# Kernel tuning notes

Hardware: AMD Instinct MI355X
Metric: run time of the kernel (lower is better)

Reference implementation:

```python
import jax, jax.numpy as jnp
import numpy as np


def setup_inputs() -> dict:
    key = jax.random.key(0)
    ks = jax.random.split(key, 4)
    B, T, C, L, DQ = 8, 2048, 256, 32, 512
    return {
        "vis_feats": jax.random.normal(ks[0], (B, T, C), dtype=jnp.float32),
        "query": jax.random.normal(ks[1], (B, L, DQ), dtype=jnp.float32),
        "W1": jax.random.normal(ks[2], (DQ, C), dtype=jnp.float32) / np.float32(np.sqrt(DQ)),
        "b1": jnp.zeros((C,), dtype=jnp.float32),
        "W2": jax.random.normal(ks[3], (DQ, C), dtype=jnp.float32) / np.float32(np.sqrt(DQ)),
        "b2": jnp.zeros((C,), dtype=jnp.float32),
        "window_size": 32,
        "num_chunks": 8,
    }


def reference(vis_feats, query, W1, b1, W2, b2, window_size, num_chunks):
    B, T, C = vis_feats.shape
    L = query.shape[1]
    # seq encoders (modeled as linear projections): [B, L, C]
    enc1 = query @ W1 + b1
    enc2 = query @ W2 + b2
    # clip-word similarity and per-clip word label: [B, T]
    sim = jnp.einsum("btc,blc->btl", vis_feats, enc1)
    clip_labels = jnp.argmax(sim, axis=2)
    NW = T - window_size + 1
    cic = window_size // num_chunks  # clips per chunk
    # sliding-window unfold indices: [NW, window_size]
    idx = jnp.arange(NW)[:, None] + jnp.arange(window_size)[None, :]
    vis_unf = vis_feats[:, idx, :]                      # [B, NW, W, C]
    lab_unf = clip_labels[:, idx].reshape(B, NW, num_chunks, cic)
    # majority vote per chunk == argmax of label histogram (ties -> smallest label,
    # matching np.bincount + np.argmax)
    counts = jax.nn.one_hot(lab_unf, L, dtype=jnp.int32).sum(axis=3)  # [B, NW, K, L]
    lbls = jnp.argmax(counts, axis=-1)                  # [B, NW, K]
    # adaptive_avg_pool3d (K, cic, C) -> (K, 1, C) == mean over clips-in-chunk
    pooled = vis_unf.reshape(B, NW, num_chunks, cic, C).mean(axis=3)  # [B, NW, K, C]
    # gather the majority-vote word encoding and modulate
    gathered = enc2[jnp.arange(B)[:, None, None], lbls]  # [B, NW, K, C]
    return gathered * pooled
```

## Files before the change

kernel.cpp:

```cpp
#include <hip/hip_runtime.h>
#include <hip/hip_bf16.h>

#define B   8
#define T   2048
#define C   256
#define L   32
#define DQ  512
#define NW  2017
#define NK  8
#define CIC 4
#define WT  32
#define SROWS (WT + (NK-1)*CIC)

__global__ __launch_bounds__(256) void enc_kernel(
    const float* __restrict__ query, const float* __restrict__ W1,
    const float* __restrict__ b1, const float* __restrict__ W2,
    const float* __restrict__ b2, float* __restrict__ enc1,
    float* __restrict__ enc2) {
  const int b = blockIdx.y, lg = blockIdx.x;
  const int c = threadIdx.x;
  __shared__ float qs[4 * DQ];
  const float* qbase = query + ((size_t)b * L + lg * 4) * DQ;
  for (int i = c; i < 4 * DQ; i += 256) qs[i] = qbase[i];
  __syncthreads();
  float a1[4] = {0.f, 0.f, 0.f, 0.f};
  float a2[4] = {0.f, 0.f, 0.f, 0.f};
  for (int d = 0; d < DQ; ++d) {
    const float w1 = W1[d * C + c];
    const float w2 = W2[d * C + c];
#pragma unroll
    for (int j = 0; j < 4; ++j) {
      a1[j] = fmaf(qs[j * DQ + d], w1, a1[j]);
      a2[j] = fmaf(qs[j * DQ + d], w2, a2[j]);
    }
  }
  const float bb1 = b1[c], bb2 = b2[c];
#pragma unroll
  for (int j = 0; j < 4; ++j) {
    const size_t o = ((size_t)b * L + lg * 4 + j) * C + c;
    enc1[o] = a1[j] + bb1;
    enc2[o] = a2[j] + bb2;
  }
}

__global__ __launch_bounds__(256) void label_kernel(
    const float* __restrict__ vis, const float* __restrict__ enc1,
    int* __restrict__ labels) {
  const int b = blockIdx.y;
  const int t0 = blockIdx.x * 64;
  const int tid = threadIdx.x;
  const int tl = tid & 63;
  const int part = tid >> 6;
  __shared__ float4 e1[L * (C / 4)];
  __shared__ float pacc[64][4 * L + 1];
  const float4* esrc = (const float4*)(enc1 + (size_t)b * L * C);
  for (int i = tid; i < L * (C / 4); i += 256) e1[i] = esrc[i];
  __syncthreads();

  const int t = t0 + tl;
  const float4* vrow = (const float4*)(vis + ((size_t)b * T + t) * C);
  float acc[L];
#pragma unroll
  for (int l = 0; l < L; ++l) acc[l] = 0.f;
  const int c4b = part * 16;
  for (int j = 0; j < 16; ++j) {
    const float4 v = vrow[c4b + j];
#pragma unroll
    for (int l = 0; l < L; ++l) {
      const float4 e = e1[l * 64 + c4b + j];
      acc[l] = fmaf(v.x, e.x, fmaf(v.y, e.y, fmaf(v.z, e.z, fmaf(v.w, e.w, acc[l]))));
    }
  }
#pragma unroll
  for (int l = 0; l < L; ++l) pacc[tl][part * L + l] = acc[l];
  __syncthreads();
  if (tid < 64) {
    float bv = -INFINITY;
    int bi = 0;
#pragma unroll
    for (int l = 0; l < L; ++l) {
      const float s = pacc[tid][l] + pacc[tid][L + l] + pacc[tid][2 * L + l] +
                      pacc[tid][3 * L + l];
      if (s > bv) { bv = s; bi = l; }
    }
    labels[(size_t)b * T + t0 + tid] = bi;
  }
}

__global__ __launch_bounds__(256) void out_kernel(
    const float* __restrict__ vis, const float* __restrict__ enc2,
    const int* __restrict__ labels, float* __restrict__ out) {
  const int b = blockIdx.y;
  const int w0 = blockIdx.x * WT;
  const int tid = threadIdx.x;
  const int lane = tid & 63;
  const int part = tid >> 6;
  __shared__ float4 S4[SROWS * (C / 4)];
  __shared__ int slbl[SROWS];

  const float4* vb = (const float4*)(vis + (size_t)b * T * C);
  const int s_begin = part * (SROWS / 4);
  {
    const int tcur = w0 + s_begin;
#define VROW(tt) vb[(size_t)((tt) > (T - 1) ? (T - 1) : (tt)) * (C / 4) + lane]
    float4 r0 = VROW(tcur), r1 = VROW(tcur + 1), r2 = VROW(tcur + 2), r3 = VROW(tcur + 3);
    for (int s = s_begin; s < s_begin + SROWS / 4; ++s) {
      float4 sum;
      sum.x = (r0.x + r1.x + r2.x + r3.x) * 0.25f;
      sum.y = (r0.y + r1.y + r2.y + r3.y) * 0.25f;
      sum.z = (r0.z + r1.z + r2.z + r3.z) * 0.25f;
      sum.w = (r0.w + r1.w + r2.w + r3.w) * 0.25f;
      S4[s * (C / 4) + lane] = sum;
      r0 = r1; r1 = r2; r2 = r3; r3 = VROW(w0 + s + 4);
    }
#undef VROW
  }

  if (tid < SROWS) {
    const int* lb = labels + (size_t)b * T;
    const int t = w0 + tid;
#define LCL(tt) lb[(tt) > (T - 1) ? (T - 1) : (tt)]
    const int l0 = LCL(t), l1 = LCL(t + 1), l2 = LCL(t + 2), l3 = LCL(t + 3);
#undef LCL
    const int c0 = 1 + (l0 == l1) + (l0 == l2) + (l0 == l3);
    const int c1 = 1 + (l1 == l0) + (l1 == l2) + (l1 == l3);
    const int c2 = 1 + (l2 == l0) + (l2 == l1) + (l2 == l3);
    const int c3 = 1 + (l3 == l0) + (l3 == l1) + (l3 == l2);
    int best = l0, bc = c0;
    if (c1 > bc || (c1 == bc && l1 < best)) { best = l1; bc = c1; }
    if (c2 > bc || (c2 == bc && l2 < best)) { best = l2; bc = c2; }
    if (c3 > bc || (c3 == bc && l3 < best)) { best = l3; bc = c3; }
    slbl[tid] = best;
  }
  __syncthreads();

  const float4* e2b = (const float4*)(enc2 + (size_t)b * L * C);
  float4* outp = (float4*)out;
  for (int i = part; i < WT * NK; i += 4) {
    const int w = i >> 3, k = i & 7;
    const int ww = w0 + w;
    if (ww >= NW) continue;
    const int s = w + CIC * k;
    const int lbl = slbl[s];
    const float4 e = e2b[lbl * (C / 4) + lane];
    const float4 sv = S4[s * (C / 4) + lane];
    float4 o;
    o.x = e.x * sv.x; o.y = e.y * sv.y; o.z = e.z * sv.z; o.w = e.w * sv.w;
    outp[(((size_t)b * NW + ww) * NK + k) * (C / 4) + lane] = o;
  }
}

extern "C" void kernel_launch(void* const* d_in, const int* in_sizes, int n_in,
                              void* d_out, int out_size, void* d_ws, size_t ws_size,
                              hipStream_t stream) {
  const float* vis   = (const float*)d_in[0];
  const float* query = (const float*)d_in[1];
  const float* W1    = (const float*)d_in[2];
  const float* b1    = (const float*)d_in[3];
  const float* W2    = (const float*)d_in[4];
  const float* b2    = (const float*)d_in[5];
  float* out = (float*)d_out;

  float* enc1 = (float*)d_ws;
  float* enc2 = enc1 + (size_t)B * L * C;
  int* labels = (int*)(enc2 + (size_t)B * L * C);

  enc_kernel<<<dim3(L / 4, B), 256, 0, stream>>>(query, W1, b1, W2, b2, enc1, enc2);
  label_kernel<<<dim3(T / 64, B), 256, 0, stream>>>(vis, enc1, labels);
  out_kernel<<<dim3((NW + WT - 1) / WT, B), 256, 0, stream>>>(vis, enc2, labels, out);
}
```

Measured before the change: 228.1 us.

## Split encoder reduction across warps, halve label tile, restructure pooling and output loops

The encoder kernel now uses 1024 threads per block, splitting the DQ reduction four ways and combining the partial sums through shared memory, which gives more parallelism to a small, latency-bound GEMM. The label kernel processes 32 timesteps per block with eight channel partitions, doubling the block count and shortening each thread's dot-product loop. The output kernel preloads all 18 rows into registers before pooling and reorders the output loop by chunk with a hoisted window bound. These changes trade more registers and shared memory for better occupancy and memory-level parallelism.

Result: faster. 217.9 us (-4.5%).

```diff
diff --git a/kernel.cpp b/kernel.cpp
--- a/kernel.cpp
+++ b/kernel.cpp
@@ -12,20 +12,25 @@
 #define WT  32
 #define SROWS (WT + (NK-1)*CIC)
 
-__global__ __launch_bounds__(256) void enc_kernel(
+__global__ __launch_bounds__(1024) void enc_kernel(
     const float* __restrict__ query, const float* __restrict__ W1,
     const float* __restrict__ b1, const float* __restrict__ W2,
     const float* __restrict__ b2, float* __restrict__ enc1,
     float* __restrict__ enc2) {
   const int b = blockIdx.y, lg = blockIdx.x;
   const int c = threadIdx.x;
+  const int q = threadIdx.y;
   __shared__ float qs[4 * DQ];
+  __shared__ float red[2][4][4][256];
   const float* qbase = query + ((size_t)b * L + lg * 4) * DQ;
-  for (int i = c; i < 4 * DQ; i += 256) qs[i] = qbase[i];
+  for (int i = q * 256 + c; i < 4 * DQ; i += 1024) qs[i] = qbase[i];
   __syncthreads();
   float a1[4] = {0.f, 0.f, 0.f, 0.f};
   float a2[4] = {0.f, 0.f, 0.f, 0.f};
-  for (int d = 0; d < DQ; ++d) {
+  const int d0 = q * (DQ / 4);
+#pragma unroll 4
+  for (int dd = 0; dd < DQ / 4; ++dd) {
+    const int d = d0 + dd;
     const float w1 = W1[d * C + c];
     const float w2 = W2[d * C + c];
 #pragma unroll
@@ -34,12 +39,21 @@
       a2[j] = fmaf(qs[j * DQ + d], w2, a2[j]);
     }
   }
-  const float bb1 = b1[c], bb2 = b2[c];
 #pragma unroll
   for (int j = 0; j < 4; ++j) {
-    const size_t o = ((size_t)b * L + lg * 4 + j) * C + c;
-    enc1[o] = a1[j] + bb1;
-    enc2[o] = a2[j] + bb2;
+    red[0][q][j][c] = a1[j];
+    red[1][q][j][c] = a2[j];
+  }
+  __syncthreads();
+  for (int o = q * 256 + c; o < 2048; o += 1024) {
+    const int e = o >> 10;
+    const int j = (o >> 8) & 3;
+    const int cc = o & 255;
+    const float v = red[e][0][j][cc] + red[e][1][j][cc] +
+                    red[e][2][j][cc] + red[e][3][j][cc];
+    const size_t off = ((size_t)b * L + lg * 4 + j) * C + cc;
+    if (e == 0) enc1[off] = v + b1[cc];
+    else        enc2[off] = v + b2[cc];
   }
 }
 
@@ -47,23 +61,23 @@
     const float* __restrict__ vis, const float* __restrict__ enc1,
     int* __restrict__ labels) {
   const int b = blockIdx.y;
-  const int t0 = blockIdx.x * 64;
+  const int t0 = blockIdx.x * 32;
   const int tid = threadIdx.x;
-  const int tl = tid & 63;
-  const int part = tid >> 6;
+  const int tl = tid & 31;
+  const int part = tid >> 5;
   __shared__ float4 e1[L * (C / 4)];
-  __shared__ float pacc[64][4 * L + 1];
+  __shared__ float pacc[32][8 * L + 1];
   const float4* esrc = (const float4*)(enc1 + (size_t)b * L * C);
   for (int i = tid; i < L * (C / 4); i += 256) e1[i] = esrc[i];
   __syncthreads();
 
-  const int t = t0 + tl;
-  const float4* vrow = (const float4*)(vis + ((size_t)b * T + t) * C);
+  const float4* vrow = (const float4*)(vis + ((size_t)b * T + t0 + tl) * C);
   float acc[L];
 #pragma unroll
   for (int l = 0; l < L; ++l) acc[l] = 0.f;
-  const int c4b = part * 16;
-  for (int j = 0; j < 16; ++j) {
+  const int c4b = part * 8;
+#pragma unroll
+  for (int j = 0; j < 8; ++j) {
     const float4 v = vrow[c4b + j];
 #pragma unroll
     for (int l = 0; l < L; ++l) {
@@ -74,13 +88,14 @@
 #pragma unroll
   for (int l = 0; l < L; ++l) pacc[tl][part * L + l] = acc[l];
   __syncthreads();
-  if (tid < 64) {
+  if (tid < 32) {
     float bv = -INFINITY;
     int bi = 0;
 #pragma unroll
     for (int l = 0; l < L; ++l) {
-      const float s = pacc[tid][l] + pacc[tid][L + l] + pacc[tid][2 * L + l] +
-                      pacc[tid][3 * L + l];
+      float s = 0.f;
+#pragma unroll
+      for (int p = 0; p < 8; ++p) s += pacc[tid][p * L + l];
       if (s > bv) { bv = s; bi = l; }
     }
     labels[(size_t)b * T + t0 + tid] = bi;
@@ -99,21 +114,24 @@
   __shared__ int slbl[SROWS];
 
   const float4* vb = (const float4*)(vis + (size_t)b * T * C);
-  const int s_begin = part * (SROWS / 4);
   {
-    const int tcur = w0 + s_begin;
-#define VROW(tt) vb[(size_t)((tt) > (T - 1) ? (T - 1) : (tt)) * (C / 4) + lane]
-    float4 r0 = VROW(tcur), r1 = VROW(tcur + 1), r2 = VROW(tcur + 2), r3 = VROW(tcur + 3);
-    for (int s = s_begin; s < s_begin + SROWS / 4; ++s) {
+    const int s_begin = part * (SROWS / 4);
+    float4 r[18];
+#pragma unroll
+    for (int j = 0; j < 18; ++j) {
+      int t = w0 + s_begin + j;
+      t = t > (T - 1) ? (T - 1) : t;
+      r[j] = vb[(size_t)t * (C / 4) + lane];
+    }
+#pragma unroll
+    for (int s = 0; s < SROWS / 4; ++s) {
       float4 sum;
-      sum.x = (r0.x + r1.x + r2.x + r3.x) * 0.25f;
-      sum.y = (r0.y + r1.y + r2.y + r3.y) * 0.25f;
-      sum.z = (r0.z + r1.z + r2.z + r3.z) * 0.25f;
-      sum.w = (r0.w + r1.w + r2.w + r3.w) * 0.25f;
-      S4[s * (C / 4) + lane] = sum;
-      r0 = r1; r1 = r2; r2 = r3; r3 = VROW(w0 + s + 4);
+      sum.x = (r[s].x + r[s + 1].x + r[s + 2].x + r[s + 3].x) * 0.25f;
+      sum.y = (r[s].y + r[s + 1].y + r[s + 2].y + r[s + 3].y) * 0.25f;
+      sum.z = (r[s].z + r[s + 1].z + r[s + 2].z + r[s + 3].z) * 0.25f;
+      sum.w = (r[s].w + r[s + 1].w + r[s + 2].w + r[s + 3].w) * 0.25f;
+      S4[(s_begin + s) * (C / 4) + lane] = sum;
     }
-#undef VROW
   }
 
   if (tid < SROWS) {
@@ -136,17 +154,20 @@
 
   const float4* e2b = (const float4*)(enc2 + (size_t)b * L * C);
   float4* outp = (float4*)out;
-  for (int i = part; i < WT * NK; i += 4) {
-    const int w = i >> 3, k = i & 7;
-    const int ww = w0 + w;
-    if (ww >= NW) continue;
-    const int s = w + CIC * k;
-    const int lbl = slbl[s];
-    const float4 e = e2b[lbl * (C / 4) + lane];
-    const float4 sv = S4[s * (C / 4) + lane];
-    float4 o;
-    o.x = e.x * sv.x; o.y = e.y * sv.y; o.z = e.z * sv.z; o.w = e.w * sv.w;
-    outp[(((size_t)b * NW + ww) * NK + k) * (C / 4) + lane] = o;
+  const int wlim = (NW - w0) < WT ? (NW - w0) : WT;
+#pragma unroll
+  for (int kk = 0; kk < 2; ++kk) {
+    const int k = part + kk * 4;
+#pragma unroll 4
+    for (int w = 0; w < wlim; ++w) {
+      const int s = w + CIC * k;
+      const int lbl = slbl[s];
+      const float4 e = e2b[lbl * (C / 4) + lane];
+      const float4 sv = S4[s * (C / 4) + lane];
+      float4 o;
+      o.x = e.x * sv.x; o.y = e.y * sv.y; o.z = e.z * sv.z; o.w = e.w * sv.w;
+      outp[(((size_t)b * NW + w0 + w) * NK + k) * (C / 4) + lane] = o;
+    }
   }
 }
 
@@ -165,7 +186,7 @@
   float* enc2 = enc1 + (size_t)B * L * C;
   int* labels = (int*)(enc2 + (size_t)B * L * C);
 
-  enc_kernel<<<dim3(L / 4, B), 256, 0, stream>>>(query, W1, b1, W2, b2, enc1, enc2);
-  label_kernel<<<dim3(T / 64, B), 256, 0, stream>>>(vis, enc1, labels);
+  enc_kernel<<<dim3(L / 4, B), dim3(256, 4), 0, stream>>>(query, W1, b1, W2, b2, enc1, enc2);
+  label_kernel<<<dim3(T / 32, B), 256, 0, stream>>>(vis, enc1, labels);
   out_kernel<<<dim3((NW + WT - 1) / WT, B), 256, 0, stream>>>(vis, enc2, labels, out);
 }
```
